# Kernel tuning notes

Hardware: AMD Instinct MI355X
Metric: run time of the kernel (lower is better)

## Reference

```python
import jax, jax.numpy as jnp
import numpy as np


def setup_inputs() -> dict:
    key = jax.random.key(0)
    ks = jax.random.split(key, 8)
    B, N, C, O = 128, 256, 512, 256
    return {
        "adjacent": jax.random.uniform(ks[0], (B, N, N), dtype=jnp.float32),
        "annotations": jax.random.normal(ks[1], (B, N, C), dtype=jnp.float32),
        "gc_bias": jax.random.normal(ks[2], (1, 1, C), dtype=jnp.float32) * 0.02,
        "gru_W": jax.random.normal(ks[3], (C, 3 * C), dtype=jnp.float32) * 0.02,
        "gru_U": jax.random.normal(ks[4], (C, 3 * C), dtype=jnp.float32) * 0.02,
        "gru_b": jax.random.normal(ks[5], (2, 3 * C), dtype=jnp.float32) * 0.02,
        "dense_W": jax.random.normal(ks[6], (C, O), dtype=jnp.float32) * 0.02,
        "dense_b": jnp.zeros((O,), dtype=jnp.float32),
    }


def reference(adjacent, annotations, gc_bias, gru_W, gru_U, gru_b, dense_W, dense_b):
    B, N, C = annotations.shape
    # GraphConvolution: per-graph adjacency matmul + bias  -> [B, N, C]
    msg = jnp.einsum('bij,bjc->bic', adjacent, annotations) + gc_bias
    # Single-step GRU (Keras GRU, reset_after=True): input = msg, state = annotations
    x = msg.reshape(-1, C)            # [B*N, C]
    h = annotations.reshape(-1, C)    # [B*N, C]
    gx = x @ gru_W + gru_b[0]         # [B*N, 3C]
    gh = h @ gru_U + gru_b[1]         # [B*N, 3C]
    xz, xr, xh = jnp.split(gx, 3, axis=-1)
    hz, hr, hh = jnp.split(gh, 3, axis=-1)
    z = jax.nn.sigmoid(xz + hz)
    r = jax.nn.sigmoid(xr + hr)
    hcand = jnp.tanh(xh + r * hh)
    hnew = z * h + (1.0 - z) * hcand  # [B*N, C]
    out = hnew.reshape(B, N, C)
    # Final Dense: in_channel -> out_channel
    return out @ dense_W + dense_b
```

## Files before the change

kernel.cpp:

```cpp
#include <hip/hip_runtime.h>

typedef __bf16 bf16;
typedef __bf16 bf16x8 __attribute__((ext_vector_type(8)));
typedef __bf16 bf16x4 __attribute__((ext_vector_type(4)));
typedef float  f32x4  __attribute__((ext_vector_type(4)));

#define NB    128
#define NN    256
#define CC    512
#define OO    256

__device__ __forceinline__ void gl_lds16(const void* g, void* l) {
  __builtin_amdgcn_global_load_lds((const __attribute__((address_space(1))) void*)g,
                                   (__attribute__((address_space(3))) void*)l, 16, 0, 0);
}

__device__ __forceinline__ float sigm_f(float x) {
  x = fminf(fmaxf(x, -30.f), 30.f);
  return 1.f / (1.f + __expf(-x));
}
__device__ __forceinline__ float tanh_f(float x) {
  x = fminf(fmaxf(x, -15.f), 15.f);
  float e = __expf(2.f * x);
  return (e - 1.f) / (e + 1.f);
}

__global__ void k_conv(const float* __restrict__ src, bf16* __restrict__ dst, int n4) {
  int stride = gridDim.x * blockDim.x;
  for (int i = blockIdx.x * blockDim.x + threadIdx.x; i < n4; i += stride) {
    float4 v = reinterpret_cast<const float4*>(src)[i];
    bf16x4 o;
    o[0] = (bf16)v.x; o[1] = (bf16)v.y; o[2] = (bf16)v.z; o[3] = (bf16)v.w;
    reinterpret_cast<bf16x4*>(dst)[i] = o;
  }
}

__global__ __launch_bounds__(256) void k_annprep(const float* __restrict__ src,
                                                 bf16* __restrict__ dB, bf16* __restrict__ dT) {
  __shared__ bf16 t[64][66];
  int b = blockIdx.z;
  const float* s = src + (size_t)b * NN * CC;
  bf16* db_ = dB + (size_t)b * NN * CC;
  bf16* dt_ = dT + (size_t)b * NN * CC;
  int j0 = blockIdx.x * 64, i0 = blockIdx.y * 64;
  int tj = threadIdx.x & 63, t4 = threadIdx.x >> 6;
  #pragma unroll
  for (int p = 0; p < 16; ++p) {
    int i = p * 4 + t4;
    bf16 bv = (bf16)s[(size_t)(i0 + i) * CC + j0 + tj];
    t[i][tj] = bv;
    db_[(size_t)(i0 + i) * CC + j0 + tj] = bv;
  }
  __syncthreads();
  #pragma unroll
  for (int p = 0; p < 16; ++p) {
    int j = p * 4 + t4;
    dt_[(size_t)(j0 + j) * NN + i0 + tj] = t[tj][j];
  }
}

__global__ __launch_bounds__(256) void k_tconv(const float* __restrict__ src, bf16* __restrict__ dst,
                                               int rows, int cols) {
  __shared__ bf16 t[64][66];
  const float* s = src;
  bf16* d = dst;
  int j0 = blockIdx.x * 64, i0 = blockIdx.y * 64;
  int tj = threadIdx.x & 63, t4 = threadIdx.x >> 6;
  #pragma unroll
  for (int p = 0; p < 16; ++p) {
    int i = p * 4 + t4;
    t[i][tj] = (bf16)s[(size_t)(i0 + i) * cols + j0 + tj];
  }
  __syncthreads();
  #pragma unroll
  for (int p = 0; p < 16; ++p) {
    int j = p * 4 + t4;
    d[(size_t)(j0 + j) * rows + i0 + tj] = t[tj][j];
  }
}

__global__ __launch_bounds__(256) void k_msg(const bf16* __restrict__ adjB,
                                             const bf16* __restrict__ annT,
                                             const float* __restrict__ gcb,
                                             bf16* __restrict__ msgB) {
  __shared__ bf16 As[128 * 64];
  __shared__ bf16 Bs[128 * 64];
  int bid = blockIdx.x;
  int b = bid >> 3, mt = (bid >> 2) & 1, nt = bid & 3;
  int tid = threadIdx.x, lane = tid & 63, wid = tid >> 6;
  int wr = wid >> 1, wc = wid & 1;
  int l15 = lane & 15, ks = lane >> 4;
  f32x4 acc[4][4] = {};
  const bf16* Ab = adjB + (size_t)b * NN * NN + (size_t)mt * 128 * NN;
  const bf16* Bb = annT + (size_t)b * CC * NN + (size_t)nt * 128 * NN;
  for (int kt = 0; kt < NN / 64; ++kt) {
    if (kt) __syncthreads();
    #pragma unroll
    for (int it = 0; it < 4; ++it) {
      int chunk = it * 256 + tid;
      int row = chunk >> 3, cc = chunk & 7;
      int sc = cc ^ (row & 7);
      gl_lds16(Ab + (size_t)row * NN + kt * 64 + sc * 8, &As[chunk * 8]);
    }
    #pragma unroll
    for (int it = 0; it < 4; ++it) {
      int chunk = it * 256 + tid;
      int row = chunk >> 3, cc = chunk & 7;
      int sc = cc ^ (row & 7);
      gl_lds16(Bb + (size_t)row * NN + kt * 64 + sc * 8, &Bs[chunk * 8]);
    }
    __syncthreads();
    #pragma unroll
    for (int kk = 0; kk < 2; ++kk) {
      bf16x8 a[4], bb[4];
      #pragma unroll
      for (int mi = 0; mi < 4; ++mi) {
        int row = wr * 64 + mi * 16 + l15;
        int ch = (kk * 4 + ks) ^ (row & 7);
        a[mi] = *(const bf16x8*)&As[row * 64 + ch * 8];
      }
      #pragma unroll
      for (int ni = 0; ni < 4; ++ni) {
        int n = wc * 64 + ni * 16 + l15;
        int ch = (kk * 4 + ks) ^ (n & 7);
        bb[ni] = *(const bf16x8*)&Bs[n * 64 + ch * 8];
      }
      #pragma unroll
      for (int mi = 0; mi < 4; ++mi)
        #pragma unroll
        for (int ni = 0; ni < 4; ++ni)
          acc[mi][ni] = __builtin_amdgcn_mfma_f32_16x16x32_bf16(a[mi], bb[ni], acc[mi][ni], 0, 0, 0);
    }
  }
  int rg = lane >> 4, cl = lane & 15;
  #pragma unroll
  for (int mi = 0; mi < 4; ++mi)
    #pragma unroll
    for (int ni = 0; ni < 4; ++ni) {
      int c = nt * 128 + wc * 64 + ni * 16 + cl;
      float g = gcb[c];
      #pragma unroll
      for (int r = 0; r < 4; ++r) {
        int R = mt * 128 + wr * 64 + mi * 16 + rg * 4 + r;
        msgB[(size_t)(b * NN + R) * CC + c] = (bf16)(acc[mi][ni][r] + g);
      }
    }
}

__global__ __launch_bounds__(512, 4) void k_gru(const bf16* __restrict__ msgB,
                                                const bf16* __restrict__ annB,
                                                const float* __restrict__ annF,
                                                const bf16* __restrict__ Wt,
                                                const bf16* __restrict__ Ut,
                                                const float* __restrict__ grub,
                                                bf16* __restrict__ hnewB) {
  __shared__ bf16 Am[128 * 32];
  __shared__ bf16 Ah[128 * 32];
  __shared__ bf16 Bw[3 * 64 * 32];
  __shared__ bf16 Bu[3 * 64 * 32];
  int bid = blockIdx.x;
  int cb = bid & 7, mb = bid >> 3;
  int c0 = cb * 64;
  int tid = threadIdx.x, lane = tid & 63, wid = tid >> 6;
  int wr = wid >> 1, wc = wid & 1;
  int l15 = lane & 15, ks = lane >> 4;
  f32x4 acc[6][2][2] = {};
  int ar = tid >> 2, ac = tid & 3;
  int asc = ac ^ ((ar >> 1) & 3);
  size_t aoff0 = (size_t)(mb * 128 + ar) * CC + asc * 8;
  int b1nr = tid >> 2, b1c = tid & 3;
  int b1g = b1nr >> 6, b1n = b1nr & 63;
  int b1sc = b1c ^ ((b1n >> 1) & 3);
  size_t b1off0 = (size_t)(b1g * CC + c0 + b1n) * CC + b1sc * 8;
  int t2 = tid & 255;
  int b2nr = (512 + t2) >> 2, b2c = t2 & 3;
  int b2g = b2nr >> 6, b2n = b2nr & 63;
  int b2sc = b2c ^ ((b2n >> 1) & 3);
  size_t b2off0 = (size_t)(b2g * CC + c0 + b2n) * CC + b2sc * 8;
  for (int kt = 0; kt < CC / 32; ++kt) {
    if (kt) __syncthreads();
    {
      size_t ko = (size_t)kt * 32;
      gl_lds16(msgB + aoff0 + ko, &Am[tid * 8]);
      gl_lds16(annB + aoff0 + ko, &Ah[tid * 8]);
      gl_lds16(Wt + b1off0 + ko, &Bw[tid * 8]);
      gl_lds16(Ut + b1off0 + ko, &Bu[tid * 8]);
      if (tid < 256) {
        gl_lds16(Wt + b2off0 + ko, &Bw[(512 + t2) * 8]);
        gl_lds16(Ut + b2off0 + ko, &Bu[(512 + t2) * 8]);
      }
    }
    __syncthreads();
    bf16x8 am[2], ah[2];
    #pragma unroll
    for (int mi = 0; mi < 2; ++mi) {
      int row = wr * 32 + mi * 16 + l15;
      int off = row * 32 + ((ks ^ ((row >> 1) & 3)) << 3);
      am[mi] = *(const bf16x8*)&Am[off];
      ah[mi] = *(const bf16x8*)&Ah[off];
    }
    #pragma unroll
    for (int g = 0; g < 3; ++g) {
      bf16x8 bw[2], bu[2];
      #pragma unroll
      for (int ni = 0; ni < 2; ++ni) {
        int n = wc * 32 + ni * 16 + l15;
        int off = g * 2048 + n * 32 + ((ks ^ ((n >> 1) & 3)) << 3);
        bw[ni] = *(const bf16x8*)&Bw[off];
        bu[ni] = *(const bf16x8*)&Bu[off];
      }
      #pragma unroll
      for (int mi = 0; mi < 2; ++mi)
        #pragma unroll
        for (int ni = 0; ni < 2; ++ni) {
          acc[g][mi][ni]     = __builtin_amdgcn_mfma_f32_16x16x32_bf16(am[mi], bw[ni], acc[g][mi][ni], 0, 0, 0);
          acc[3 + g][mi][ni] = __builtin_amdgcn_mfma_f32_16x16x32_bf16(ah[mi], bu[ni], acc[3 + g][mi][ni], 0, 0, 0);
        }
    }
  }
  int rg = lane >> 4, cl = lane & 15;
  const float* b0 = grub;
  const float* b1 = grub + 3 * CC;
  #pragma unroll
  for (int mi = 0; mi < 2; ++mi)
    #pragma unroll
    for (int ni = 0; ni < 2; ++ni) {
      int c = c0 + wc * 32 + ni * 16 + cl;
      float bz = b0[c] + b1[c];
      float br = b0[CC + c] + b1[CC + c];
      float bh0 = b0[2 * CC + c], bh1 = b1[2 * CC + c];
      #pragma unroll
      for (int r = 0; r < 4; ++r) {
        int R = mb * 128 + wr * 32 + mi * 16 + rg * 4 + r;
        float z  = sigm_f(acc[0][mi][ni][r] + acc[3][mi][ni][r] + bz);
        float rr = sigm_f(acc[1][mi][ni][r] + acc[4][mi][ni][r] + br);
        float hc = tanh_f(acc[2][mi][ni][r] + bh0 + rr * (acc[5][mi][ni][r] + bh1));
        float h  = annF[(size_t)R * CC + c];
        hnewB[(size_t)R * CC + c] = (bf16)(z * h + (1.f - z) * hc);
      }
    }
}

__global__ __launch_bounds__(256) void k_out(const bf16* __restrict__ hB,
                                             const bf16* __restrict__ DWt,
                                             const float* __restrict__ db,
                                             float* __restrict__ out) {
  __shared__ bf16 As[128 * 64];
  __shared__ bf16 Bs[128 * 64];
  int bid = blockIdx.x;
  int mt = bid >> 1, nt = bid & 1;
  int tid = threadIdx.x, lane = tid & 63, wid = tid >> 6;
  int wr = wid >> 1, wc = wid & 1;
  int l15 = lane & 15, ks = lane >> 4;
  f32x4 acc[4][4] = {};
  for (int kt = 0; kt < CC / 64; ++kt) {
    if (kt) __syncthreads();
    #pragma unroll
    for (int it = 0; it < 4; ++it) {
      int chunk = it * 256 + tid;
      int row = chunk >> 3, cc = chunk & 7;
      int sc = cc ^ (row & 7);
      gl_lds16(hB + (size_t)(mt * 128 + row) * CC + kt * 64 + sc * 8, &As[chunk * 8]);
      gl_lds16(DWt + (size_t)(nt * 128 + row) * CC + kt * 64 + sc * 8, &Bs[chunk * 8]);
    }
    __syncthreads();
    #pragma unroll
    for (int kk = 0; kk < 2; ++kk) {
      bf16x8 a[4], bb[4];
      #pragma unroll
      for (int mi = 0; mi < 4; ++mi) {
        int row = wr * 64 + mi * 16 + l15;
        int ch = (kk * 4 + ks) ^ (row & 7);
        a[mi] = *(const bf16x8*)&As[row * 64 + ch * 8];
      }
      #pragma unroll
      for (int ni = 0; ni < 4; ++ni) {
        int n = wc * 64 + ni * 16 + l15;
        int ch = (kk * 4 + ks) ^ (n & 7);
        bb[ni] = *(const bf16x8*)&Bs[n * 64 + ch * 8];
      }
      #pragma unroll
      for (int mi = 0; mi < 4; ++mi)
        #pragma unroll
        for (int ni = 0; ni < 4; ++ni)
          acc[mi][ni] = __builtin_amdgcn_mfma_f32_16x16x32_bf16(a[mi], bb[ni], acc[mi][ni], 0, 0, 0);
    }
  }
  int rg = lane >> 4, cl = lane & 15;
  #pragma unroll
  for (int mi = 0; mi < 4; ++mi)
    #pragma unroll
    for (int ni = 0; ni < 4; ++ni) {
      int c = nt * 128 + wc * 64 + ni * 16 + cl;
      float g = db[c];
      #pragma unroll
      for (int r = 0; r < 4; ++r) {
        int R = mt * 128 + wr * 64 + mi * 16 + rg * 4 + r;
        out[(size_t)R * OO + c] = acc[mi][ni][r] + g;
      }
    }
}

extern "C" void kernel_launch(void* const* d_in, const int* in_sizes, int n_in,
                              void* d_out, int out_size, void* d_ws, size_t ws_size,
                              hipStream_t stream) {
  const float* adj = (const float*)d_in[0];
  const float* ann = (const float*)d_in[1];
  const float* gcb = (const float*)d_in[2];
  const float* gW  = (const float*)d_in[3];
  const float* gU  = (const float*)d_in[4];
  const float* gb  = (const float*)d_in[5];
  const float* dW  = (const float*)d_in[6];
  const float* db  = (const float*)d_in[7];
  float* out = (float*)d_out;
  char* ws = (char*)d_ws;
  bf16* annB  = (bf16*)(ws + 0);
  bf16* adjB  = (bf16*)(ws + 33554432);
  bf16* hnewB = (bf16*)(ws + 33554432);
  bf16* annT  = (bf16*)(ws + 50331648);
  bf16* msgB  = (bf16*)(ws + 83886080);
  bf16* WtB   = (bf16*)(ws + 117440512);
  bf16* UtB   = (bf16*)(ws + 119013376);
  bf16* DWtB  = (bf16*)(ws + 120586240);

  hipLaunchKernelGGL(k_conv, dim3(1024), dim3(256), 0, stream, adj, adjB, 8388608 / 4);
  hipLaunchKernelGGL(k_annprep, dim3(8, 4, 128), dim3(256), 0, stream, ann, annB, annT);
  hipLaunchKernelGGL(k_tconv, dim3(24, 8, 1), dim3(256), 0, stream, gW, WtB, 512, 1536);
  hipLaunchKernelGGL(k_tconv, dim3(24, 8, 1), dim3(256), 0, stream, gU, UtB, 512, 1536);
  hipLaunchKernelGGL(k_tconv, dim3(4, 8, 1), dim3(256), 0, stream, dW, DWtB, 512, 256);
  hipLaunchKernelGGL(k_msg, dim3(1024), dim3(256), 0, stream, adjB, annT, gcb, msgB);
  hipLaunchKernelGGL(k_gru, dim3(2048), dim3(512), 0, stream, msgB, annB, ann, WtB, UtB, gb, hnewB);
  hipLaunchKernelGGL(k_out, dim3(512), dim3(256), 0, stream, hnewB, DWtB, db, out);
}
```

Before: 348.2 us.

## Double-buffer LDS tiles in all GEMM kernels and raise MFMA wave priority

```diff
diff --git a/kernel.cpp b/kernel.cpp
--- a/kernel.cpp
+++ b/kernel.cpp
@@ -62,20 +62,18 @@
 __global__ __launch_bounds__(256) void k_tconv(const float* __restrict__ src, bf16* __restrict__ dst,
                                                int rows, int cols) {
   __shared__ bf16 t[64][66];
-  const float* s = src;
-  bf16* d = dst;
   int j0 = blockIdx.x * 64, i0 = blockIdx.y * 64;
   int tj = threadIdx.x & 63, t4 = threadIdx.x >> 6;
   #pragma unroll
   for (int p = 0; p < 16; ++p) {
     int i = p * 4 + t4;
-    t[i][tj] = (bf16)s[(size_t)(i0 + i) * cols + j0 + tj];
+    t[i][tj] = (bf16)src[(size_t)(i0 + i) * cols + j0 + tj];
   }
   __syncthreads();
   #pragma unroll
   for (int p = 0; p < 16; ++p) {
     int j = p * 4 + t4;
-    d[(size_t)(j0 + j) * rows + i0 + tj] = t[tj][j];
+    dst[(size_t)(j0 + j) * rows + i0 + tj] = t[tj][j];
   }
 }
 
@@ -83,8 +81,8 @@
                                              const bf16* __restrict__ annT,
                                              const float* __restrict__ gcb,
                                              bf16* __restrict__ msgB) {
-  __shared__ bf16 As[128 * 64];
-  __shared__ bf16 Bs[128 * 64];
+  __shared__ bf16 As[2][128 * 32];
+  __shared__ bf16 Bs[2][128 * 32];
   int bid = blockIdx.x;
   int b = bid >> 3, mt = (bid >> 2) & 1, nt = bid & 3;
   int tid = threadIdx.x, lane = tid & 63, wid = tid >> 6;
@@ -93,44 +91,43 @@
   f32x4 acc[4][4] = {};
   const bf16* Ab = adjB + (size_t)b * NN * NN + (size_t)mt * 128 * NN;
   const bf16* Bb = annT + (size_t)b * CC * NN + (size_t)nt * 128 * NN;
-  for (int kt = 0; kt < NN / 64; ++kt) {
-    if (kt) __syncthreads();
-    #pragma unroll
-    for (int it = 0; it < 4; ++it) {
-      int chunk = it * 256 + tid;
-      int row = chunk >> 3, cc = chunk & 7;
-      int sc = cc ^ (row & 7);
-      gl_lds16(Ab + (size_t)row * NN + kt * 64 + sc * 8, &As[chunk * 8]);
-    }
-    #pragma unroll
-    for (int it = 0; it < 4; ++it) {
-      int chunk = it * 256 + tid;
-      int row = chunk >> 3, cc = chunk & 7;
-      int sc = cc ^ (row & 7);
-      gl_lds16(Bb + (size_t)row * NN + kt * 64 + sc * 8, &Bs[chunk * 8]);
-    }
+  int r0 = tid >> 2, ch0 = tid & 3;
+  int sc0 = ch0 ^ ((r0 >> 1) & 3);
+  int r1 = 64 + r0;
+  int sc1 = ch0 ^ ((r1 >> 1) & 3);
+  auto STAGE = [&](int buf, int kt) {
+    int ko = kt * 32;
+    gl_lds16(Ab + (size_t)r0 * NN + ko + sc0 * 8, &As[buf][tid * 8]);
+    gl_lds16(Ab + (size_t)r1 * NN + ko + sc1 * 8, &As[buf][(256 + tid) * 8]);
+    gl_lds16(Bb + (size_t)r0 * NN + ko + sc0 * 8, &Bs[buf][tid * 8]);
+    gl_lds16(Bb + (size_t)r1 * NN + ko + sc1 * 8, &Bs[buf][(256 + tid) * 8]);
+  };
+  STAGE(0, 0);
+  __syncthreads();
+  for (int kt = 0; kt < NN / 32; ++kt) {
+    int p = kt & 1;
+    if (kt < NN / 32 - 1) STAGE(p ^ 1, kt + 1);
+    bf16x8 a[4], bb[4];
+    #pragma unroll
+    for (int mi = 0; mi < 4; ++mi) {
+      int row = wr * 64 + mi * 16 + l15;
+      int off = row * 32 + ((ks ^ ((row >> 1) & 3)) << 3);
+      a[mi] = *(const bf16x8*)&As[p][off];
+    }
+    #pragma unroll
+    for (int ni = 0; ni < 4; ++ni) {
+      int n = wc * 64 + ni * 16 + l15;
+      int off = n * 32 + ((ks ^ ((n >> 1) & 3)) << 3);
+      bb[ni] = *(const bf16x8*)&Bs[p][off];
+    }
+    __builtin_amdgcn_s_setprio(1);
+    #pragma unroll
+    for (int mi = 0; mi < 4; ++mi)
+      #pragma unroll
+      for (int ni = 0; ni < 4; ++ni)
+        acc[mi][ni] = __builtin_amdgcn_mfma_f32_16x16x32_bf16(a[mi], bb[ni], acc[mi][ni], 0, 0, 0);
+    __builtin_amdgcn_s_setprio(0);
     __syncthreads();
-    #pragma unroll
-    for (int kk = 0; kk < 2; ++kk) {
-      bf16x8 a[4], bb[4];
-      #pragma unroll
-      for (int mi = 0; mi < 4; ++mi) {
-        int row = wr * 64 + mi * 16 + l15;
-        int ch = (kk * 4 + ks) ^ (row & 7);
-        a[mi] = *(const bf16x8*)&As[row * 64 + ch * 8];
-      }
-      #pragma unroll
-      for (int ni = 0; ni < 4; ++ni) {
-        int n = wc * 64 + ni * 16 + l15;
-        int ch = (kk * 4 + ks) ^ (n & 7);
-        bb[ni] = *(const bf16x8*)&Bs[n * 64 + ch * 8];
-      }
-      #pragma unroll
-      for (int mi = 0; mi < 4; ++mi)
-        #pragma unroll
-        for (int ni = 0; ni < 4; ++ni)
-          acc[mi][ni] = __builtin_amdgcn_mfma_f32_16x16x32_bf16(a[mi], bb[ni], acc[mi][ni], 0, 0, 0);
-    }
   }
   int rg = lane >> 4, cl = lane & 15;
   #pragma unroll
@@ -149,15 +146,14 @@
 
 __global__ __launch_bounds__(512, 4) void k_gru(const bf16* __restrict__ msgB,
                                                 const bf16* __restrict__ annB,
-                                                const float* __restrict__ annF,
                                                 const bf16* __restrict__ Wt,
                                                 const bf16* __restrict__ Ut,
                                                 const float* __restrict__ grub,
                                                 bf16* __restrict__ hnewB) {
-  __shared__ bf16 Am[128 * 32];
-  __shared__ bf16 Ah[128 * 32];
-  __shared__ bf16 Bw[3 * 64 * 32];
-  __shared__ bf16 Bu[3 * 64 * 32];
+  __shared__ bf16 Am[2][128 * 32];
+  __shared__ bf16 Ah[2][128 * 32];
+  __shared__ bf16 Bw[2][3 * 64 * 32];
+  __shared__ bf16 Bu[2][3 * 64 * 32];
   int bid = blockIdx.x;
   int cb = bid & 7, mb = bid >> 3;
   int c0 = cb * 64;
@@ -177,27 +173,31 @@
   int b2g = b2nr >> 6, b2n = b2nr & 63;
   int b2sc = b2c ^ ((b2n >> 1) & 3);
   size_t b2off0 = (size_t)(b2g * CC + c0 + b2n) * CC + b2sc * 8;
+
+  auto STAGE = [&](int buf, int kt) {
+    size_t ko = (size_t)kt * 32;
+    gl_lds16(msgB + aoff0 + ko, &Am[buf][tid * 8]);
+    gl_lds16(annB + aoff0 + ko, &Ah[buf][tid * 8]);
+    gl_lds16(Wt + b1off0 + ko, &Bw[buf][tid * 8]);
+    gl_lds16(Ut + b1off0 + ko, &Bu[buf][tid * 8]);
+    if (tid < 256) {
+      gl_lds16(Wt + b2off0 + ko, &Bw[buf][(512 + t2) * 8]);
+      gl_lds16(Ut + b2off0 + ko, &Bu[buf][(512 + t2) * 8]);
+    }
+  };
+
+  STAGE(0, 0);
+  __syncthreads();
   for (int kt = 0; kt < CC / 32; ++kt) {
-    if (kt) __syncthreads();
-    {
-      size_t ko = (size_t)kt * 32;
-      gl_lds16(msgB + aoff0 + ko, &Am[tid * 8]);
-      gl_lds16(annB + aoff0 + ko, &Ah[tid * 8]);
-      gl_lds16(Wt + b1off0 + ko, &Bw[tid * 8]);
-      gl_lds16(Ut + b1off0 + ko, &Bu[tid * 8]);
-      if (tid < 256) {
-        gl_lds16(Wt + b2off0 + ko, &Bw[(512 + t2) * 8]);
-        gl_lds16(Ut + b2off0 + ko, &Bu[(512 + t2) * 8]);
-      }
-    }
-    __syncthreads();
+    int p = kt & 1;
+    if (kt < CC / 32 - 1) STAGE(p ^ 1, kt + 1);
     bf16x8 am[2], ah[2];
     #pragma unroll
     for (int mi = 0; mi < 2; ++mi) {
       int row = wr * 32 + mi * 16 + l15;
       int off = row * 32 + ((ks ^ ((row >> 1) & 3)) << 3);
-      am[mi] = *(const bf16x8*)&Am[off];
-      ah[mi] = *(const bf16x8*)&Ah[off];
+      am[mi] = *(const bf16x8*)&Am[p][off];
+      ah[mi] = *(const bf16x8*)&Ah[p][off];
     }
     #pragma unroll
     for (int g = 0; g < 3; ++g) {
@@ -206,9 +206,10 @@
       for (int ni = 0; ni < 2; ++ni) {
         int n = wc * 32 + ni * 16 + l15;
         int off = g * 2048 + n * 32 + ((ks ^ ((n >> 1) & 3)) << 3);
-        bw[ni] = *(const bf16x8*)&Bw[off];
-        bu[ni] = *(const bf16x8*)&Bu[off];
-      }
+        bw[ni] = *(const bf16x8*)&Bw[p][off];
+        bu[ni] = *(const bf16x8*)&Bu[p][off];
+      }
+      __builtin_amdgcn_s_setprio(1);
       #pragma unroll
       for (int mi = 0; mi < 2; ++mi)
         #pragma unroll
@@ -216,7 +217,9 @@
           acc[g][mi][ni]     = __builtin_amdgcn_mfma_f32_16x16x32_bf16(am[mi], bw[ni], acc[g][mi][ni], 0, 0, 0);
           acc[3 + g][mi][ni] = __builtin_amdgcn_mfma_f32_16x16x32_bf16(ah[mi], bu[ni], acc[3 + g][mi][ni], 0, 0, 0);
         }
-    }
+      __builtin_amdgcn_s_setprio(0);
+    }
+    __syncthreads();
   }
   int rg = lane >> 4, cl = lane & 15;
   const float* b0 = grub;
@@ -235,7 +238,7 @@
         float z  = sigm_f(acc[0][mi][ni][r] + acc[3][mi][ni][r] + bz);
         float rr = sigm_f(acc[1][mi][ni][r] + acc[4][mi][ni][r] + br);
         float hc = tanh_f(acc[2][mi][ni][r] + bh0 + rr * (acc[5][mi][ni][r] + bh1));
-        float h  = annF[(size_t)R * CC + c];
+        float h  = (float)annB[(size_t)R * CC + c];
         hnewB[(size_t)R * CC + c] = (bf16)(z * h + (1.f - z) * hc);
       }
     }
@@ -245,25 +248,29 @@
                                              const bf16* __restrict__ DWt,
                                              const float* __restrict__ db,
                                              float* __restrict__ out) {
-  __shared__ bf16 As[128 * 64];
-  __shared__ bf16 Bs[128 * 64];
+  __shared__ bf16 As[2][128 * 64];
+  __shared__ bf16 Bs[2][128 * 64];
   int bid = blockIdx.x;
   int mt = bid >> 1, nt = bid & 1;
   int tid = threadIdx.x, lane = tid & 63, wid = tid >> 6;
   int wr = wid >> 1, wc = wid & 1;
   int l15 = lane & 15, ks = lane >> 4;
   f32x4 acc[4][4] = {};
-  for (int kt = 0; kt < CC / 64; ++kt) {
-    if (kt) __syncthreads();
+  auto STAGE = [&](int buf, int kt) {
     #pragma unroll
     for (int it = 0; it < 4; ++it) {
       int chunk = it * 256 + tid;
       int row = chunk >> 3, cc = chunk & 7;
       int sc = cc ^ (row & 7);
-      gl_lds16(hB + (size_t)(mt * 128 + row) * CC + kt * 64 + sc * 8, &As[chunk * 8]);
-      gl_lds16(DWt + (size_t)(nt * 128 + row) * CC + kt * 64 + sc * 8, &Bs[chunk * 8]);
-    }
-    __syncthreads();
+      gl_lds16(hB + (size_t)(mt * 128 + row) * CC + kt * 64 + sc * 8, &As[buf][chunk * 8]);
+      gl_lds16(DWt + (size_t)(nt * 128 + row) * CC + kt * 64 + sc * 8, &Bs[buf][chunk * 8]);
+    }
+  };
+  STAGE(0, 0);
+  __syncthreads();
+  for (int kt = 0; kt < CC / 64; ++kt) {
+    int p = kt & 1;
+    if (kt < CC / 64 - 1) STAGE(p ^ 1, kt + 1);
     #pragma unroll
     for (int kk = 0; kk < 2; ++kk) {
       bf16x8 a[4], bb[4];
@@ -271,20 +278,23 @@
       for (int mi = 0; mi < 4; ++mi) {
         int row = wr * 64 + mi * 16 + l15;
         int ch = (kk * 4 + ks) ^ (row & 7);
-        a[mi] = *(const bf16x8*)&As[row * 64 + ch * 8];
+        a[mi] = *(const bf16x8*)&As[p][row * 64 + ch * 8];
       }
       #pragma unroll
       for (int ni = 0; ni < 4; ++ni) {
         int n = wc * 64 + ni * 16 + l15;
         int ch = (kk * 4 + ks) ^ (n & 7);
-        bb[ni] = *(const bf16x8*)&Bs[n * 64 + ch * 8];
-      }
+        bb[ni] = *(const bf16x8*)&Bs[p][n * 64 + ch * 8];
+      }
+      __builtin_amdgcn_s_setprio(1);
       #pragma unroll
       for (int mi = 0; mi < 4; ++mi)
         #pragma unroll
         for (int ni = 0; ni < 4; ++ni)
           acc[mi][ni] = __builtin_amdgcn_mfma_f32_16x16x32_bf16(a[mi], bb[ni], acc[mi][ni], 0, 0, 0);
-    }
+      __builtin_amdgcn_s_setprio(0);
+    }
+    __syncthreads();
   }
   int rg = lane >> 4, cl = lane & 15;
   #pragma unroll
@@ -329,6 +339,6 @@
   hipLaunchKernelGGL(k_tconv, dim3(24, 8, 1), dim3(256), 0, stream, gU, UtB, 512, 1536);
   hipLaunchKernelGGL(k_tconv, dim3(4, 8, 1), dim3(256), 0, stream, dW, DWtB, 512, 256);
   hipLaunchKernelGGL(k_msg, dim3(1024), dim3(256), 0, stream, adjB, annT, gcb, msgB);
-  hipLaunchKernelGGL(k_gru, dim3(2048), dim3(512), 0, stream, msgB, annB, ann, WtB, UtB, gb, hnewB);
+  hipLaunchKernelGGL(k_gru, dim3(2048), dim3(512), 0, stream, msgB, annB, WtB, UtB, gb, hnewB);
   hipLaunchKernelGGL(k_out, dim3(512), dim3(256), 0, stream, hnewB, DWtB, db, out);
 }
```

Result: slower. 904.6 us (+159.8%).
